# Kernel tuning notes

Measured on AMD Instinct MI355X. Metric: run time of the kernel, lower is better.

Reference implementation:

```python
import jax, jax.numpy as jnp
import numpy as np

D = 1024        # d_model
H = 16          # n_heads
DF = 4096       # d_ff
MAXL = 1024     # max_len
MAXSTEPS = 24   # max_steps


def setup_inputs() -> dict:
    key = jax.random.key(0)
    ks = jax.random.split(key, 10)
    B, S = 4, 1024
    s = 0.02
    f32 = jnp.float32
    return {
        "x": jax.random.normal(ks[0], (B, S, D), f32),
        "original_input": jax.random.normal(ks[1], (B, S, D), f32),
        "think_step": 5,
        "step_embed": jax.random.normal(ks[2], (MAXSTEPS, D), f32) * s,
        "Wqkv": jax.random.normal(ks[3], (D, 3 * D), f32) * s,
        "bqkv": jnp.zeros((3 * D,), f32),
        "Wout": jax.random.normal(ks[4], (D, D), f32) * s,
        "bout": jnp.zeros((D,), f32),
        "Wg": jax.random.normal(ks[5], (2 * D, D), f32) * s,
        "bg": jnp.zeros((D,), f32),
        "rel_pos_bias": jax.random.normal(ks[6], (2 * MAXL - 1,), f32) * s,
        "W1": jax.random.normal(ks[7], (D, DF), f32) * s,
        "b1": jnp.zeros((DF,), f32),
        "W2": jax.random.normal(ks[8], (DF, D), f32) * s,
        "b2": jnp.zeros((D,), f32),
        "ln1_g": jnp.ones((D,), f32),
        "ln1_b": jnp.zeros((D,), f32),
        "ln2_g": jnp.ones((D,), f32),
        "ln2_b": jnp.zeros((D,), f32),
    }


def _layer_norm(x, g, b, eps=1e-5):
    m = jnp.mean(x, axis=-1, keepdims=True)
    v = jnp.mean((x - m) ** 2, axis=-1, keepdims=True)
    return (x - m) * jax.lax.rsqrt(v + eps) * g + b


def reference(x, original_input, think_step, step_embed, Wqkv, bqkv, Wout, bout,
              Wg, bg, rel_pos_bias, W1, b1, W2, b2, ln1_g, ln1_b, ln2_g, ln2_b):
    B, S, _ = x.shape
    hd = D // H
    # gated residual input injection
    gate = jax.nn.sigmoid(jnp.concatenate([x, original_input], axis=-1) @ Wg + bg)
    x = x * (1.0 - gate) + original_input * gate
    # think-step embedding (clamped)
    step = min(int(think_step), MAXSTEPS - 1)
    x = x + step_embed[step][None, None, :]
    # qkv projection -> (3, B, H, S, hd)
    qkv = (x @ Wqkv + bqkv).reshape(B, S, 3, H, hd).transpose(2, 0, 3, 1, 4)
    q, k, v = qkv[0], qkv[1], qkv[2]
    scores = jnp.einsum('bhqd,bhkd->bhqk', q, k) * (hd ** -0.5)
    # relative position bias: dist clamped to [0, 2*MAXL-2]
    pos = jnp.arange(S)
    rel = jnp.clip(pos[:, None] - pos[None, :] + (MAXL - 1), 0, 2 * MAXL - 2)
    scores = scores + rel_pos_bias[rel][None, None]  # (B,H,S,S)
    probs = jax.nn.softmax(scores, axis=-1)
    attn = jnp.einsum('bhqk,bhkd->bhqd', probs, v)
    attn = attn.transpose(0, 2, 1, 3).reshape(B, S, D)
    attn = attn @ Wout + bout
    x = _layer_norm(x + attn, ln1_g, ln1_b)
    h = jax.nn.gelu(x @ W1 + b1, approximate=False) @ W2 + b2
    return _layer_norm(x + h, ln2_g, ln2_b)
```

## Files before the change

### kernel.cpp

```cpp
#include <hip/hip_runtime.h>
#include <hip/hip_bf16.h>
#include <math.h>

#define D_MODEL 1024
#define NH      16
#define HD      64
#define DFF     4096
#define SEQ     1024
#define BATCH   4
#define TOK     (BATCH*SEQ)
#define MAXSTEPS 24

typedef __hip_bfloat16 bf16;
typedef __attribute__((ext_vector_type(8))) short short8;
typedef __attribute__((ext_vector_type(4))) float floatx4;

__device__ __forceinline__ float b2f(bf16 v){ return __bfloat162float(v); }
__device__ __forceinline__ bf16  f2b(float v){ return __float2bfloat16(v); }

__device__ __forceinline__ void gload_lds16(const bf16* g, bf16* l){
    __builtin_amdgcn_global_load_lds((const __attribute__((address_space(1))) void*)g,
                                     (__attribute__((address_space(3))) void*)l, 16, 0, 0);
}

template<int TN, int EPI>
__global__ __launch_bounds__(256)
void mfma_gemm(const bf16* __restrict__ A, const bf16* __restrict__ Bt,
               const float* __restrict__ bias, void* __restrict__ outv,
               int M, int N, int K)
{
    constexpr int NT  = TN / 32;
    constexpr int NBP = TN / 64;
    constexpr int R   = (TN == 64) ? 4 : 3;
    __shared__ bf16 As[R][128 * 32];
    __shared__ bf16 Bs[R][TN * 32];
    const int tid  = threadIdx.x;
    const int lane = tid & 63;
    const int w    = tid >> 6;
    const int wm   = w & 1, wn = w >> 1;
    const int fr   = lane & 15;
    const int q    = lane >> 4;

    const int tn_g = gridDim.x;
    const int nwg  = tn_g * gridDim.y;
    const int bid  = blockIdx.y * tn_g + blockIdx.x;
    const int o    = (bid & 7) * (nwg >> 3) + (bid >> 3);
    const int bandw = 8 * tn_g;
    const int band  = o / bandw;
    const int rr    = o - band * bandw;
    const int row0 = (band * 8 + (rr & 7)) * 128;
    const int col0 = (rr >> 3) * TN;

    const bf16* gA[2]; int sA_[2];
    #pragma unroll
    for (int p = 0; p < 2; ++p) {
        int s  = p * 256 + tid;
        int m  = s >> 2;
        int qg = (s & 3) ^ ((m >> 1) & 3);
        gA[p]  = A + (size_t)(row0 + m) * K + qg * 8;
        sA_[p] = s * 8;
    }
    const bf16* gB[NBP]; int sB_[NBP];
    #pragma unroll
    for (int p = 0; p < NBP; ++p) {
        int s  = p * 256 + tid;
        int m  = s >> 2;
        int qg = (s & 3) ^ ((m >> 1) & 3);
        gB[p]  = Bt + (size_t)(col0 + m) * K + qg * 8;
        sB_[p] = s * 8;
    }

    int aoff[4], boff[NT];
    #pragma unroll
    for (int t = 0; t < 4; ++t) {
        int ml  = wm * 64 + t * 16 + fr;
        aoff[t] = (ml * 4 + (q ^ ((ml >> 1) & 3))) * 8;
    }
    #pragma unroll
    for (int t = 0; t < NT; ++t) {
        int nl  = wn * (TN / 2) + t * 16 + fr;
        boff[t] = (nl * 4 + (q ^ ((nl >> 1) & 3))) * 8;
    }

    #pragma unroll
    for (int pt = 0; pt < R - 1; ++pt) {
        #pragma unroll
        for (int p = 0; p < 2; ++p)   gload_lds16(gA[p] + pt * 32, &As[pt][sA_[p]]);
        #pragma unroll
        for (int p = 0; p < NBP; ++p) gload_lds16(gB[p] + pt * 32, &Bs[pt][sB_[p]]);
    }

    floatx4 acc[4][NT] = {};
    const int nk = K >> 5;
    int cur = 0;
    int kst = (R - 1) * 32;

    for (int t = 0; t < nk; ++t) {
        if constexpr (TN == 64) asm volatile("s_waitcnt vmcnt(6)" ::: "memory");
        else                    asm volatile("s_waitcnt vmcnt(4)" ::: "memory");
        __builtin_amdgcn_s_barrier();
        asm volatile("" ::: "memory");

        if (kst < K) {
            int sb = (cur == 0) ? (R - 1) : (cur - 1);
            #pragma unroll
            for (int p = 0; p < 2; ++p)   gload_lds16(gA[p] + kst, &As[sb][sA_[p]]);
            #pragma unroll
            for (int p = 0; p < NBP; ++p) gload_lds16(gB[p] + kst, &Bs[sb][sB_[p]]);
            kst += 32;
        }

        short8 af[4], bfg[NT];
        #pragma unroll
        for (int i = 0; i < 4; ++i)  af[i]  = *(const short8*)(&As[cur][aoff[i]]);
        #pragma unroll
        for (int j = 0; j < NT; ++j) bfg[j] = *(const short8*)(&Bs[cur][boff[j]]);
        #pragma unroll
        for (int i = 0; i < 4; ++i)
            #pragma unroll
            for (int j = 0; j < NT; ++j)
                acc[i][j] = __builtin_amdgcn_mfma_f32_16x16x32_bf16(af[i], bfg[j], acc[i][j], 0, 0, 0);

        cur = (cur == R - 1) ? 0 : (cur + 1);
    }

    float bv[NT];
    #pragma unroll
    for (int nt = 0; nt < NT; ++nt) bv[nt] = bias[col0 + wn * (TN / 2) + nt * 16 + fr];
    #pragma unroll
    for (int mt = 0; mt < 4; ++mt) {
        #pragma unroll
        for (int nt = 0; nt < NT; ++nt) {
            int col = col0 + wn * (TN / 2) + nt * 16 + fr;
            #pragma unroll
            for (int r = 0; r < 4; ++r) {
                int row = row0 + wm * 64 + mt * 16 + q * 4 + r;
                float v = acc[mt][nt][r] + bv[nt];
                if (EPI == 0) {
                    ((float*)outv)[(size_t)row * N + col] = v;
                } else if (EPI == 1) {
                    ((bf16*)outv)[(size_t)row * N + col] = f2b(v);
                } else {
                    float g = 0.5f * v * (1.0f + erff(v * 0.70710678118654752f));
                    ((bf16*)outv)[(size_t)row * N + col] = f2b(g);
                }
            }
        }
    }
}

__global__ __launch_bounds__(256)
void transpose_kernel(const float* __restrict__ W, bf16* __restrict__ WT,
                      int K, int N)
{
    __shared__ float t[32][33];
    const int tx = threadIdx.x & 31, ty = threadIdx.x >> 5;
    const int n0 = blockIdx.x * 32, k0 = blockIdx.y * 32;
    #pragma unroll
    for (int i = 0; i < 4; ++i)
        t[ty + i * 8][tx] = W[(size_t)(k0 + ty + i * 8) * N + n0 + tx];
    __syncthreads();
    #pragma unroll
    for (int i = 0; i < 4; ++i)
        WT[(size_t)(n0 + ty + i * 8) * K + k0 + tx] = f2b(t[tx][ty + i * 8]);
}

__global__ __launch_bounds__(256)
void vtrans_kernel(const bf16* __restrict__ qkv, bf16* __restrict__ Vt)
{
    __shared__ float t[32][33];
    const int blk = blockIdx.x;
    const int dt = blk & 1;
    const int st = (blk >> 1) & 31;
    const int h  = (blk >> 6) & 15;
    const int b  = blk >> 10;
    const int tx = threadIdx.x & 31, ty = threadIdx.x >> 5;
    #pragma unroll
    for (int i = 0; i < 4; ++i)
        t[ty + i * 8][tx] = b2f(qkv[(size_t)(b * SEQ + st * 32 + ty + i * 8) * 3072
                                    + 2048 + h * 64 + dt * 32 + tx]);
    __syncthreads();
    #pragma unroll
    for (int i = 0; i < 4; ++i)
        Vt[(size_t)((b * NH + h) * 64 + dt * 32 + ty + i * 8) * SEQ + st * 32 + tx]
            = f2b(t[tx][ty + i * 8]);
}

__global__ __launch_bounds__(256)
void xcat_kernel(const float* __restrict__ x, const float* __restrict__ orig,
                 bf16* __restrict__ xcat)
{
    int i = blockIdx.x * 256 + threadIdx.x;
    float4 xv = ((const float4*)x)[i];
    float4 ov = ((const float4*)orig)[i];
    int t = i >> 8, c4 = (i & 255) * 4;
    bf16* px = xcat + (size_t)t * 2048 + c4;
    px[0] = f2b(xv.x); px[1] = f2b(xv.y); px[2] = f2b(xv.z); px[3] = f2b(xv.w);
    bf16* po = px + 1024;
    po[0] = f2b(ov.x); po[1] = f2b(ov.y); po[2] = f2b(ov.z); po[3] = f2b(ov.w);
}

__global__ __launch_bounds__(256)
void gatemix_kernel(const float* __restrict__ x, const float* __restrict__ orig,
                    const float* __restrict__ z, const int* __restrict__ step_ptr,
                    const float* __restrict__ se, bf16* __restrict__ xw)
{
    int i = blockIdx.x * 256 + threadIdx.x;
    int st = step_ptr[0];
    st = st < 0 ? 0 : (st > MAXSTEPS - 1 ? MAXSTEPS - 1 : st);
    float g = 1.0f / (1.0f + expf(-z[i]));
    float v = x[i] * (1.0f - g) + orig[i] * g + se[st * D_MODEL + (i & 1023)];
    xw[i] = f2b(v);
}

__global__ __launch_bounds__(256)
void fattn_kernel(const bf16* __restrict__ qkv, const bf16* __restrict__ Vt,
                  const float* __restrict__ relb, bf16* __restrict__ out)
{
    __shared__ bf16 KPs[128 * 64];
    __shared__ bf16 Vs [64 * 128];
    __shared__ float relb_s[1088];

    const int tid  = threadIdx.x;
    const int lane = tid & 63;
    const int w    = tid >> 6;
    const int fr   = lane & 15;
    const int quad = lane >> 4;

    const int qt = blockIdx.x & 15;
    const int h  = (blockIdx.x >> 4) & 15;
    const int b  = blockIdx.x >> 8;
    const int bq = b * SEQ;
    const int bh = b * NH + h;

    for (int i = tid; i < 1087; i += 256)
        relb_s[i] = relb[qt * 64 + i] - 8.0f;

    const int qrow = bq + qt * 64 + w * 16 + fr;
    short8 qf[2];
    {
        const bf16* qp = qkv + (size_t)qrow * 3072 + h * 64 + quad * 8;
        qf[0] = *(const short8*)(qp);
        qf[1] = *(const short8*)(qp + 32);
    }

    int ibase[4];
    #pragma unroll
    for (int r = 0; r < 4; ++r)
        ibase[r] = (w * 16 + quad * 4 + r) - fr + 1023;

    float lsum[4] = {0.f, 0.f, 0.f, 0.f};
    floatx4 accO[4];
    #pragma unroll
    for (int nt = 0; nt < 4; ++nt) accO[nt] = (floatx4){0.f, 0.f, 0.f, 0.f};

    for (int k0 = 0; k0 < SEQ; k0 += 128) {
        __syncthreads();
        #pragma unroll
        for (int it = 0; it < 4; ++it) {
            int s = it * 256 + tid;
            int key = s >> 3, cs = s & 7;
            int c = cs ^ (key & 7);
            const bf16* src = qkv + (size_t)(bq + k0 + key) * 3072 + 1024 + h * 64 + c * 8;
            gload_lds16(src, KPs + (size_t)s * 8);
        }
        #pragma unroll
        for (int it = 0; it < 4; ++it) {
            int s = it * 256 + tid;
            int row = s >> 4, cs = s & 15;
            int c = cs ^ (row & 15);
            const bf16* src = Vt + (size_t)(bh * 64 + row) * SEQ + k0 + c * 8;
            gload_lds16(src, Vs + (size_t)s * 8);
        }
        __syncthreads();

        floatx4 accS[8];
        #pragma unroll
        for (int t = 0; t < 8; ++t) accS[t] = (floatx4){0.f, 0.f, 0.f, 0.f};
        __builtin_amdgcn_s_setprio(1);
        #pragma unroll
        for (int t = 0; t < 8; ++t) {
            int row = t * 16 + fr;
            #pragma unroll
            for (int ks = 0; ks < 2; ++ks) {
                int slot = (ks * 4 + quad) ^ (row & 7);
                short8 kf = *(const short8*)(KPs + (size_t)row * 64 + slot * 8);
                accS[t] = __builtin_amdgcn_mfma_f32_16x16x32_bf16(qf[ks], kf, accS[t], 0, 0, 0);
            }
        }
        __builtin_amdgcn_s_setprio(0);

        __syncthreads();

        bf16* Ps = KPs + w * 2048;
        #pragma unroll
        for (int t = 0; t < 8; ++t) {
            int keyl = t * 16 + fr;
            int cbase = keyl >> 3, koff = keyl & 7;
            #pragma unroll
            for (int r = 0; r < 4; ++r) {
                float bias = relb_s[ibase[r] - k0 - t * 16];
                float p = __expf(fmaf(accS[t][r], 0.125f, bias));
                lsum[r] += p;
                int row = quad * 4 + r;
                int slot = cbase ^ (row & 15);
                Ps[(size_t)row * 128 + slot * 8 + koff] = f2b(p);
            }
        }

        __builtin_amdgcn_s_setprio(1);
        #pragma unroll
        for (int ks = 0; ks < 4; ++ks) {
            int slotp = (ks * 4 + quad) ^ (fr & 15);
            short8 pf = *(const short8*)(Ps + (size_t)fr * 128 + slotp * 8);
            #pragma unroll
            for (int nt = 0; nt < 4; ++nt) {
                int vrow = nt * 16 + fr;
                int slotv = (ks * 4 + quad) ^ (vrow & 15);
                short8 vf = *(const short8*)(Vs + (size_t)vrow * 128 + slotv * 8);
                accO[nt] = __builtin_amdgcn_mfma_f32_16x16x32_bf16(pf, vf, accO[nt], 0, 0, 0);
            }
        }
        __builtin_amdgcn_s_setprio(0);
    }

    float inv[4];
    #pragma unroll
    for (int r = 0; r < 4; ++r) {
        float v = lsum[r];
        v += __shfl_xor(v, 1); v += __shfl_xor(v, 2);
        v += __shfl_xor(v, 4); v += __shfl_xor(v, 8);
        inv[r] = 1.0f / v;
    }

    #pragma unroll
    for (int nt = 0; nt < 4; ++nt) {
        int col = h * 64 + nt * 16 + fr;
        #pragma unroll
        for (int r = 0; r < 4; ++r) {
            int t = bq + qt * 64 + w * 16 + quad * 4 + r;
            out[(size_t)t * D_MODEL + col] = f2b(accO[nt][r] * inv[r]);
        }
    }
}

template<bool OUT_BF16>
__global__ __launch_bounds__(256)
void ln_kernel(const bf16* __restrict__ a, const float* __restrict__ add,
               const float* __restrict__ g, const float* __restrict__ bb,
               void* __restrict__ outv)
{
    __shared__ float red[256];
    __shared__ float red2[256];
    const int row = blockIdx.x;
    const int tid = threadIdx.x;
    float s[4];
    float lsum = 0.f, lsq = 0.f;
    #pragma unroll
    for (int u = 0; u < 4; ++u) {
        int i = tid + 256 * u;
        float v = b2f(a[row * D_MODEL + i]) + add[row * D_MODEL + i];
        s[u] = v; lsum += v; lsq += v * v;
    }
    red[tid] = lsum; red2[tid] = lsq; __syncthreads();
    for (int s2 = 128; s2 > 0; s2 >>= 1) {
        if (tid < s2) { red[tid] += red[tid + s2]; red2[tid] += red2[tid + s2]; }
        __syncthreads();
    }
    float mean = red[0] * (1.0f / D_MODEL);
    float var  = red2[0] * (1.0f / D_MODEL) - mean * mean;
    float rs = rsqrtf(var + 1e-5f);
    #pragma unroll
    for (int u = 0; u < 4; ++u) {
        int i = tid + 256 * u;
        float o = (s[u] - mean) * rs * g[i] + bb[i];
        if (OUT_BF16) ((bf16*)outv)[row * D_MODEL + i] = f2b(o);
        else          ((float*)outv)[row * D_MODEL + i] = o;
    }
}

extern "C" void kernel_launch(void* const* d_in, const int* in_sizes, int n_in,
                              void* d_out, int out_size, void* d_ws, size_t ws_size,
                              hipStream_t stream)
{
    const float* x     = (const float*)d_in[0];
    const float* orig  = (const float*)d_in[1];
    const int*   step  = (const int*)  d_in[2];
    const float* se    = (const float*)d_in[3];
    const float* Wqkv  = (const float*)d_in[4];
    const float* bqkv  = (const float*)d_in[5];
    const float* Wout  = (const float*)d_in[6];
    const float* bout  = (const float*)d_in[7];
    const float* Wg    = (const float*)d_in[8];
    const float* bg    = (const float*)d_in[9];
    const float* relb  = (const float*)d_in[10];
    const float* W1    = (const float*)d_in[11];
    const float* b1    = (const float*)d_in[12];
    const float* W2    = (const float*)d_in[13];
    const float* b2    = (const float*)d_in[14];
    const float* ln1g  = (const float*)d_in[15];
    const float* ln1b  = (const float*)d_in[16];
    const float* ln2g  = (const float*)d_in[17];
    const float* ln2b  = (const float*)d_in[18];

    char* ws = (char*)d_ws;
    bf16* WgT   = (bf16*)(ws);
    bf16* WqkvT = (bf16*)(ws + ( 4u << 20));
    bf16* WoutT = (bf16*)(ws + (10u << 20));
    bf16* W1T   = (bf16*)(ws + (12u << 20));
    bf16* W2T   = (bf16*)(ws + (20u << 20));
    bf16* xcat  = (bf16*)(ws + (28u << 20));
    bf16* xw    = (bf16*)(ws + (28u << 20));
    bf16* attnb = (bf16*)(ws + (36u << 20));
    bf16* qkvb  = (bf16*)(ws + (44u << 20));
    bf16* Vt    = (bf16*)(ws + (68u << 20));
    bf16* h     = (bf16*)(ws + (44u << 20));
    float* tmp  = (float*)d_out;

    dim3 blk(256);

    transpose_kernel<<<dim3(1024/32, 2048/32), blk, 0, stream>>>(Wg,   WgT,   2048, 1024);
    transpose_kernel<<<dim3(3072/32, 1024/32), blk, 0, stream>>>(Wqkv, WqkvT, 1024, 3072);
    transpose_kernel<<<dim3(1024/32, 1024/32), blk, 0, stream>>>(Wout, WoutT, 1024, 1024);
    transpose_kernel<<<dim3(4096/32, 1024/32), blk, 0, stream>>>(W1,   W1T,   1024, 4096);
    transpose_kernel<<<dim3(1024/32, 4096/32), blk, 0, stream>>>(W2,   W2T,   4096, 1024);
    xcat_kernel<<<TOK, blk, 0, stream>>>(x, orig, xcat);

    mfma_gemm<64, 0><<<dim3(D_MODEL/64, TOK/128), blk, 0, stream>>>(
        xcat, WgT, bg, tmp, TOK, D_MODEL, 2*D_MODEL);

    gatemix_kernel<<<TOK*D_MODEL/256, blk, 0, stream>>>(x, orig, tmp, step, se, xw);

    mfma_gemm<128, 1><<<dim3(3*D_MODEL/128, TOK/128), blk, 0, stream>>>(
        xw, WqkvT, bqkv, qkvb, TOK, 3*D_MODEL, D_MODEL);

    vtrans_kernel<<<BATCH*NH*64, blk, 0, stream>>>(qkvb, Vt);

    fattn_kernel<<<BATCH*NH*(SEQ/64), blk, 0, stream>>>(qkvb, Vt, relb, attnb);

    mfma_gemm<64, 0><<<dim3(D_MODEL/64, TOK/128), blk, 0, stream>>>(
        attnb, WoutT, bout, tmp, TOK, D_MODEL, D_MODEL);

    ln_kernel<true><<<TOK, blk, 0, stream>>>(xw, tmp, ln1g, ln1b, xw);

    mfma_gemm<128, 2><<<dim3(DFF/128, TOK/128), blk, 0, stream>>>(
        xw, W1T, b1, h, TOK, DFF, D_MODEL);

    mfma_gemm<64, 0><<<dim3(D_MODEL/64, TOK/128), blk, 0, stream>>>(
        h, W2T, b2, tmp, TOK, D_MODEL, DFF);

    ln_kernel<false><<<TOK, blk, 0, stream>>>(xw, tmp, ln2g, ln2b, d_out);
}
```

Before: 464.3 us.

## Fuse gate-mix into gate GEMM, merge weight transposes, split-K the W2 GEMM

The sigmoid gate mix and step-embedding add move into a new epilogue of the gate GEMM. This drops the standalone gatemix kernel and the fp32 round-trip of the gate logits. The five weight-transpose launches become a single launch that picks its matrix by block index. The W2 GEMM now uses 128-wide tiles with a two-way split-K; the second partial goes to a workspace buffer and is summed inside the final layer norm. That adds an extra fp32 partial write and read, and workspace buffers are relocated to make room.

Result: faster. 430.2 us (-7.3%).

```diff
diff --git a/kernel.cpp b/kernel.cpp
--- a/kernel.cpp
+++ b/kernel.cpp
@@ -23,11 +23,14 @@
                                      (__attribute__((address_space(3))) void*)l, 16, 0, 0);
 }
 
-template<int TN, int EPI>
+template<int TN, int EPI, bool SPLITK>
 __global__ __launch_bounds__(256)
 void mfma_gemm(const bf16* __restrict__ A, const bf16* __restrict__ Bt,
                const float* __restrict__ bias, void* __restrict__ outv,
-               int M, int N, int K)
+               void* __restrict__ outv2,
+               int M, int N, int K, int lda, int ldb,
+               const float* __restrict__ xg, const float* __restrict__ og,
+               const float* __restrict__ seg, const int* __restrict__ stepp)
 {
     constexpr int NT  = TN / 32;
     constexpr int NBP = TN / 64;
@@ -41,6 +44,12 @@
     const int fr   = lane & 15;
     const int q    = lane >> 4;
 
+    if (SPLITK) {
+        int z = blockIdx.z;
+        A  += (size_t)z * K;
+        Bt += (size_t)z * K;
+    }
+
     const int tn_g = gridDim.x;
     const int nwg  = tn_g * gridDim.y;
     const int bid  = blockIdx.y * tn_g + blockIdx.x;
@@ -57,7 +66,7 @@
         int s  = p * 256 + tid;
         int m  = s >> 2;
         int qg = (s & 3) ^ ((m >> 1) & 3);
-        gA[p]  = A + (size_t)(row0 + m) * K + qg * 8;
+        gA[p]  = A + (size_t)(row0 + m) * lda + qg * 8;
         sA_[p] = s * 8;
     }
     const bf16* gB[NBP]; int sB_[NBP];
@@ -66,7 +75,7 @@
         int s  = p * 256 + tid;
         int m  = s >> 2;
         int qg = (s & 3) ^ ((m >> 1) & 3);
-        gB[p]  = Bt + (size_t)(col0 + m) * K + qg * 8;
+        gB[p]  = Bt + (size_t)(col0 + m) * ldb + qg * 8;
         sB_[p] = s * 8;
     }
 
@@ -124,9 +133,23 @@
         cur = (cur == R - 1) ? 0 : (cur + 1);
     }
 
-    float bv[NT];
-    #pragma unroll
-    for (int nt = 0; nt < NT; ++nt) bv[nt] = bias[col0 + wn * (TN / 2) + nt * 16 + fr];
+    void* outp = outv;
+    float bscale = 1.0f;
+    if (SPLITK && blockIdx.z != 0) { outp = outv2; bscale = 0.0f; }
+
+    int st = 0;
+    if (EPI == 3) {
+        st = stepp[0];
+        st = st < 0 ? 0 : (st > MAXSTEPS - 1 ? MAXSTEPS - 1 : st);
+    }
+
+    float bv[NT], sv[NT];
+    #pragma unroll
+    for (int nt = 0; nt < NT; ++nt) {
+        int col = col0 + wn * (TN / 2) + nt * 16 + fr;
+        bv[nt] = bias[col] * bscale;
+        if (EPI == 3) sv[nt] = seg[st * D_MODEL + col];
+    }
     #pragma unroll
     for (int mt = 0; mt < 4; ++mt) {
         #pragma unroll
@@ -137,25 +160,44 @@
                 int row = row0 + wm * 64 + mt * 16 + q * 4 + r;
                 float v = acc[mt][nt][r] + bv[nt];
                 if (EPI == 0) {
-                    ((float*)outv)[(size_t)row * N + col] = v;
+                    ((float*)outp)[(size_t)row * N + col] = v;
                 } else if (EPI == 1) {
-                    ((bf16*)outv)[(size_t)row * N + col] = f2b(v);
+                    ((bf16*)outp)[(size_t)row * N + col] = f2b(v);
+                } else if (EPI == 2) {
+                    float g = 0.5f * v * (1.0f + erff(v * 0.70710678118654752f));
+                    ((bf16*)outp)[(size_t)row * N + col] = f2b(g);
                 } else {
-                    float g = 0.5f * v * (1.0f + erff(v * 0.70710678118654752f));
-                    ((bf16*)outv)[(size_t)row * N + col] = f2b(g);
+                    float g = 1.0f / (1.0f + __expf(-v));
+                    size_t idx = (size_t)row * N + col;
+                    float mix = xg[idx] * (1.0f - g) + og[idx] * g + sv[nt];
+                    ((bf16*)outp)[idx] = f2b(mix);
                 }
             }
         }
     }
 }
 
-__global__ __launch_bounds__(256)
-void transpose_kernel(const float* __restrict__ W, bf16* __restrict__ WT,
-                      int K, int N)
+#define NTRANS_BLOCKS 14336
+__global__ __launch_bounds__(256)
+void transpose_all_kernel(const float* __restrict__ Wg,   bf16* __restrict__ WgT,
+                          const float* __restrict__ Wqkv, bf16* __restrict__ WqkvT,
+                          const float* __restrict__ Wout, bf16* __restrict__ WoutT,
+                          const float* __restrict__ W1,   bf16* __restrict__ W1T,
+                          const float* __restrict__ W2,   bf16* __restrict__ W2T)
 {
     __shared__ float t[32][33];
+    const int bid = blockIdx.x;
+    if (bid >= NTRANS_BLOCKS) return;
+    const float* W; bf16* WT; int K, N, base;
+    if      (bid <  2048) { W = Wg;   WT = WgT;   K = 2048; N = 1024; base = 0; }
+    else if (bid <  5120) { W = Wqkv; WT = WqkvT; K = 1024; N = 3072; base = 2048; }
+    else if (bid <  6144) { W = Wout; WT = WoutT; K = 1024; N = 1024; base = 5120; }
+    else if (bid < 10240) { W = W1;   WT = W1T;   K = 1024; N = 4096; base = 6144; }
+    else                  { W = W2;   WT = W2T;   K = 4096; N = 1024; base = 10240; }
+    const int lb  = bid - base;
+    const int ntx = N >> 5;
+    const int n0 = (lb % ntx) * 32, k0 = (lb / ntx) * 32;
     const int tx = threadIdx.x & 31, ty = threadIdx.x >> 5;
-    const int n0 = blockIdx.x * 32, k0 = blockIdx.y * 32;
     #pragma unroll
     for (int i = 0; i < 4; ++i)
         t[ty + i * 8][tx] = W[(size_t)(k0 + ty + i * 8) * N + n0 + tx];
@@ -201,19 +243,6 @@
 }
 
 __global__ __launch_bounds__(256)
-void gatemix_kernel(const float* __restrict__ x, const float* __restrict__ orig,
-                    const float* __restrict__ z, const int* __restrict__ step_ptr,
-                    const float* __restrict__ se, bf16* __restrict__ xw)
-{
-    int i = blockIdx.x * 256 + threadIdx.x;
-    int st = step_ptr[0];
-    st = st < 0 ? 0 : (st > MAXSTEPS - 1 ? MAXSTEPS - 1 : st);
-    float g = 1.0f / (1.0f + expf(-z[i]));
-    float v = x[i] * (1.0f - g) + orig[i] * g + se[st * D_MODEL + (i & 1023)];
-    xw[i] = f2b(v);
-}
-
-__global__ __launch_bounds__(256)
 void fattn_kernel(const bf16* __restrict__ qkv, const bf16* __restrict__ Vt,
                   const float* __restrict__ relb, bf16* __restrict__ out)
 {
@@ -344,9 +373,10 @@
     }
 }
 
-template<bool OUT_BF16>
+template<bool OUT_BF16, bool HAS2>
 __global__ __launch_bounds__(256)
 void ln_kernel(const bf16* __restrict__ a, const float* __restrict__ add,
+               const float* __restrict__ add2,
                const float* __restrict__ g, const float* __restrict__ bb,
                void* __restrict__ outv)
 {
@@ -360,6 +390,7 @@
     for (int u = 0; u < 4; ++u) {
         int i = tid + 256 * u;
         float v = b2f(a[row * D_MODEL + i]) + add[row * D_MODEL + i];
+        if (HAS2) v += add2[row * D_MODEL + i];
         s[u] = v; lsum += v; lsq += v * v;
     }
     red[tid] = lsum; red2[tid] = lsq; __syncthreads();
@@ -409,45 +440,46 @@
     bf16* WoutT = (bf16*)(ws + (10u << 20));
     bf16* W1T   = (bf16*)(ws + (12u << 20));
     bf16* W2T   = (bf16*)(ws + (20u << 20));
-    bf16* xcat  = (bf16*)(ws + (28u << 20));
     bf16* xw    = (bf16*)(ws + (28u << 20));
+    bf16* xcat  = (bf16*)(ws + (36u << 20));
     bf16* attnb = (bf16*)(ws + (36u << 20));
-    bf16* qkvb  = (bf16*)(ws + (44u << 20));
-    bf16* Vt    = (bf16*)(ws + (68u << 20));
     bf16* h     = (bf16*)(ws + (44u << 20));
+    bf16* qkvb  = (bf16*)(ws + (52u << 20));
+    float* tmp2 = (float*)(ws);
+    bf16* Vt    = (bf16*)d_out;
     float* tmp  = (float*)d_out;
 
     dim3 blk(256);
 
-    transpose_kernel<<<dim3(1024/32, 2048/32), blk, 0, stream>>>(Wg,   WgT,   2048, 1024);
-    transpose_kernel<<<dim3(3072/32, 1024/32), blk, 0, stream>>>(Wqkv, WqkvT, 1024, 3072);
-    transpose_kernel<<<dim3(1024/32, 1024/32), blk, 0, stream>>>(Wout, WoutT, 1024, 1024);
-    transpose_kernel<<<dim3(4096/32, 1024/32), blk, 0, stream>>>(W1,   W1T,   1024, 4096);
-    transpose_kernel<<<dim3(1024/32, 4096/32), blk, 0, stream>>>(W2,   W2T,   4096, 1024);
+    transpose_all_kernel<<<NTRANS_BLOCKS, blk, 0, stream>>>(Wg, WgT, Wqkv, WqkvT,
+                                                    Wout, WoutT, W1, W1T, W2, W2T);
     xcat_kernel<<<TOK, blk, 0, stream>>>(x, orig, xcat);
 
-    mfma_gemm<64, 0><<<dim3(D_MODEL/64, TOK/128), blk, 0, stream>>>(
-        xcat, WgT, bg, tmp, TOK, D_MODEL, 2*D_MODEL);
-
-    gatemix_kernel<<<TOK*D_MODEL/256, blk, 0, stream>>>(x, orig, tmp, step, se, xw);
-
-    mfma_gemm<128, 1><<<dim3(3*D_MODEL/128, TOK/128), blk, 0, stream>>>(
-        xw, WqkvT, bqkv, qkvb, TOK, 3*D_MODEL, D_MODEL);
+    mfma_gemm<64, 3, false><<<dim3(D_MODEL/64, TOK/128), blk, 0, stream>>>(
+        xcat, WgT, bg, xw, nullptr, TOK, D_MODEL, 2*D_MODEL, 2*D_MODEL, 2*D_MODEL,
+        x, orig, se, step);
+
+    mfma_gemm<128, 1, false><<<dim3(3*D_MODEL/128, TOK/128), blk, 0, stream>>>(
+        xw, WqkvT, bqkv, qkvb, nullptr, TOK, 3*D_MODEL, D_MODEL, D_MODEL, D_MODEL,
+        nullptr, nullptr, nullptr, nullptr);
 
     vtrans_kernel<<<BATCH*NH*64, blk, 0, stream>>>(qkvb, Vt);
 
     fattn_kernel<<<BATCH*NH*(SEQ/64), blk, 0, stream>>>(qkvb, Vt, relb, attnb);
 
-    mfma_gemm<64, 0><<<dim3(D_MODEL/64, TOK/128), blk, 0, stream>>>(
-        attnb, WoutT, bout, tmp, TOK, D_MODEL, D_MODEL);
-
-    ln_kernel<true><<<TOK, blk, 0, stream>>>(xw, tmp, ln1g, ln1b, xw);
-
-    mfma_gemm<128, 2><<<dim3(DFF/128, TOK/128), blk, 0, stream>>>(
-        xw, W1T, b1, h, TOK, DFF, D_MODEL);
-
-    mfma_gemm<64, 0><<<dim3(D_MODEL/64, TOK/128), blk, 0, stream>>>(
-        h, W2T, b2, tmp, TOK, D_MODEL, DFF);
-
-    ln_kernel<false><<<TOK, blk, 0, stream>>>(xw, tmp, ln2g, ln2b, d_out);
-}
+    mfma_gemm<64, 0, false><<<dim3(D_MODEL/64, TOK/128), blk, 0, stream>>>(
+        attnb, WoutT, bout, tmp, nullptr, TOK, D_MODEL, D_MODEL, D_MODEL, D_MODEL,
+        nullptr, nullptr, nullptr, nullptr);
+
+    ln_kernel<true, false><<<TOK, blk, 0, stream>>>(xw, tmp, nullptr, ln1g, ln1b, xw);
+
+    mfma_gemm<128, 2, false><<<dim3(DFF/128, TOK/128), blk, 0, stream>>>(
+        xw, W1T, b1, h, nullptr, TOK, DFF, D_MODEL, D_MODEL, D_MODEL,
+        nullptr, nullptr, nullptr, nullptr);
+
+    mfma_gemm<128, 0, true><<<dim3(D_MODEL/128, TOK/128, 2), blk, 0, stream>>>(
+        h, W2T, b2, tmp, tmp2, TOK, D_MODEL, DFF/2, DFF, DFF,
+        nullptr, nullptr, nullptr, nullptr);
+
+    ln_kernel<false, true><<<TOK, blk, 0, stream>>>(xw, tmp, tmp2, ln2g, ln2b, d_out);
+}
```
